# Performance work log

Hardware: AMD Instinct MI355X
Metric: run time of the kernel (lower is better)

## Reference

```python
import jax, jax.numpy as jnp
import numpy as np

D_MODEL = 256
NHEAD = 8
HEAD_DIM = D_MODEL // NHEAD
EPS_ATTN = 1e-6
EPS_LN = 1e-5


def layer_norm(x, g, b):
    mu = jnp.mean(x, axis=-1, keepdims=True)
    var = jnp.mean(jnp.square(x - mu), axis=-1, keepdims=True)
    return (x - mu) * jax.lax.rsqrt(var + EPS_LN) * g + b


def setup_inputs() -> dict:
    key = jax.random.key(0)
    ks = jax.random.split(key, 9)
    N, L, S = 8, 8192, 8192
    d = D_MODEL
    sc = 1.0 / np.sqrt(d)
    return {
        "x": jax.random.normal(ks[0], (N, L, d), dtype=jnp.float32),
        "source": jax.random.normal(ks[1], (N, S, d), dtype=jnp.float32),
        "Wq": jax.random.normal(ks[2], (d, d), dtype=jnp.float32) * sc,
        "Wk": jax.random.normal(ks[3], (d, d), dtype=jnp.float32) * sc,
        "Wv": jax.random.normal(ks[4], (d, d), dtype=jnp.float32) * sc,
        "Wm": jax.random.normal(ks[5], (d, d), dtype=jnp.float32) * sc,
        "W1": jax.random.normal(ks[6], (2 * d, d), dtype=jnp.float32) * (1.0 / np.sqrt(2 * d)),
        "W2": jax.random.normal(ks[7], (d, d), dtype=jnp.float32) * sc,
        "g1": jnp.ones((d,), jnp.float32),
        "b1": jnp.zeros((d,), jnp.float32),
        "g2": jnp.ones((d,), jnp.float32),
        "b2": jnp.zeros((d,), jnp.float32),
    }


def linear_attention(q, k, v):
    # q: [N,L,H,D], k,v: [N,S,H,D]
    Q = jax.nn.elu(q) + 1.0
    K = jax.nn.elu(k) + 1.0
    S = v.shape[1]
    v = v / S
    KV = jnp.einsum('nshd,nshv->nhdv', K, v)          # [N,H,D,D]
    Z = 1.0 / (jnp.einsum('nlhd,nhd->nlh', Q, K.sum(axis=1)) + EPS_ATTN)
    out = jnp.einsum('nlhd,nhdv,nlh->nlhv', Q, KV, Z) * S
    return out


def reference(x, source, Wq, Wk, Wv, Wm, W1, W2, g1, b1, g2, b2):
    N, L, _ = x.shape
    q = (x @ Wq).reshape(N, L, NHEAD, HEAD_DIM)
    k = (source @ Wk).reshape(N, -1, NHEAD, HEAD_DIM)
    v = (source @ Wv).reshape(N, -1, NHEAD, HEAD_DIM)
    msg = linear_attention(q, k, v).reshape(N, L, D_MODEL)
    msg = layer_norm(msg @ Wm, g1, b1)
    msg = jnp.concatenate([x, msg], axis=2)
    msg = jax.nn.relu(msg @ W1) @ W2
    msg = layer_norm(msg, g2, b2)
    return x + msg
```

## Files before the change

### kernel.cpp

```cpp
#include <hip/hip_runtime.h>

typedef __attribute__((ext_vector_type(4))) float f32x4;
typedef __attribute__((ext_vector_type(8))) short short8;
typedef __attribute__((ext_vector_type(4))) unsigned short us4;
typedef __attribute__((ext_vector_type(8))) unsigned short us8;

#define D_MODEL 256
#define SEQ 8192L
#define NBATCH 8
#define TOTROWS 65536L

__device__ inline unsigned short f2bf(float f){
  unsigned int u = __float_as_uint(f);
  u += 0x7fffu + ((u >> 16) & 1u);
  return (unsigned short)(u >> 16);
}
__device__ inline float bf2f(unsigned short h){
  return __uint_as_float(((unsigned int)h) << 16);
}
__device__ inline f32x4 mfma16(short8 a, short8 b, f32x4 c){
  return __builtin_amdgcn_mfma_f32_16x16x32_bf16(a, b, c, 0, 0, 0);
}
__device__ inline us8 pack8(f32x4 a, f32x4 b){
  us8 o;
  o[0]=f2bf(a[0]); o[1]=f2bf(a[1]); o[2]=f2bf(a[2]); o[3]=f2bf(a[3]);
  o[4]=f2bf(b[0]); o[5]=f2bf(b[1]); o[6]=f2bf(b[2]); o[7]=f2bf(b[3]);
  return o;
}

__global__ void prep_weights(const float* __restrict__ Wq, const float* __restrict__ Wk,
                             const float* __restrict__ Wv, const float* __restrict__ Wm,
                             const float* __restrict__ W1, const float* __restrict__ W2,
                             unsigned short* __restrict__ WT){
  int o = blockIdx.x * 256 + threadIdx.x;
  int m = o >> 16, rem = o & 65535, n = rem >> 8, k = rem & 255;
  const float* s;
  switch(m){
    case 0: s = Wq; break;
    case 1: s = Wk; break;
    case 2: s = Wv; break;
    case 3: s = Wm; break;
    case 4: s = W1; break;
    case 5: s = W1 + 65536; break;
    default: s = W2; break;
  }
  WT[o] = f2bf(s[k * 256 + n]);
}

__global__ __launch_bounds__(256) void kv_proj(
    const float* __restrict__ src, const unsigned short* __restrict__ WT,
    unsigned short* __restrict__ Kw, unsigned short* __restrict__ Vw)
{
  __shared__ unsigned short As[128][40];
  __shared__ unsigned short Bs[128][40];
  const int t = threadIdx.x, lane = t & 63, wid = t >> 6;
  const int l16 = lane & 15, g4 = lane >> 4;
  const int wr = (wid >> 1) * 64, wc = (wid & 1) * 64;
  const int mb = blockIdx.x, nb = blockIdx.y;
  const long rowbase = (long)mb * 128;
  const unsigned short* Wsl = WT + (nb < 2 ? 1 : 2) * 65536 + (nb & 1) * 128 * 256;
  const int rA = t >> 1, cA = (t & 1) * 16;

  f32x4 acc[4][4] = {};
  for(int kb = 0; kb < 256; kb += 32){
    {
      const float* g = src + (rowbase + rA) * 256 + kb + cA;
      f32x4 v0 = *(const f32x4*)g;
      f32x4 v1 = *(const f32x4*)(g + 4);
      f32x4 v2 = *(const f32x4*)(g + 8);
      f32x4 v3 = *(const f32x4*)(g + 12);
      *(us8*)&As[rA][cA]     = pack8(v0, v1);
      *(us8*)&As[rA][cA + 8] = pack8(v2, v3);
      const unsigned short* wb = Wsl + rA * 256 + kb + cA;
      *(us8*)&Bs[rA][cA]     = *(const us8*)wb;
      *(us8*)&Bs[rA][cA + 8] = *(const us8*)(wb + 8);
    }
    __syncthreads();
    short8 afr[4], bfr[4];
    #pragma unroll
    for(int mi = 0; mi < 4; mi++) afr[mi] = *(const short8*)&As[wr + mi*16 + l16][g4*8];
    #pragma unroll
    for(int ni = 0; ni < 4; ni++) bfr[ni] = *(const short8*)&Bs[wc + ni*16 + l16][g4*8];
    #pragma unroll
    for(int mi = 0; mi < 4; mi++)
      #pragma unroll
      for(int ni = 0; ni < 4; ni++)
        acc[mi][ni] = mfma16(afr[mi], bfr[ni], acc[mi][ni]);
    __syncthreads();
  }

  const bool isK = nb < 2;
  unsigned short* dst = isK ? Kw : Vw;
  const int colbase = (nb & 1) * 128 + wc;
  #pragma unroll
  for(int mi = 0; mi < 4; mi++)
    #pragma unroll
    for(int ni = 0; ni < 4; ni++)
      #pragma unroll
      for(int rr = 0; rr < 4; rr++){
        long row = rowbase + wr + mi*16 + g4*4 + rr;
        int col = colbase + ni*16 + l16;
        float v = acc[mi][ni][rr];
        v = isK ? (v > 0.f ? v + 1.f : __expf(v)) : v * (1.f / 8192.f);
        dst[row * 256 + col] = f2bf(v);
      }
}

__global__ __launch_bounds__(256) void kv_acc(const unsigned short* __restrict__ Kw,
                                              const unsigned short* __restrict__ Vw,
                                              float* __restrict__ part){
  const int c = blockIdx.x;
  const int n = blockIdx.y;
  const int t = threadIdx.x;
  const int h = t >> 5, d = t & 31;
  const long base = ((long)n * SEQ + (long)c * 128) * 256;
  float acc[32];
  #pragma unroll
  for(int j = 0; j < 32; j++) acc[j] = 0.f;
  float ks = 0.f;
  for(int rr = 0; rr < 128; rr++){
    const unsigned short* Kr = Kw + base + (long)rr * 256;
    const unsigned short* Vr = Vw + base + (long)rr * 256;
    float kv = bf2f(Kr[h * 32 + d]);
    ks += kv;
    #pragma unroll
    for(int q = 0; q < 4; q++){
      us8 vv = *(const us8*)(Vr + h * 32 + q * 8);
      #pragma unroll
      for(int j = 0; j < 8; j++) acc[q*8 + j] += kv * bf2f(vv[j]);
    }
  }
  float* p = part + ((long)(n * 64 + c) * 33) * 256;
  #pragma unroll
  for(int v = 0; v < 32; v++) p[v * 256 + t] = acc[v];
  p[32 * 256 + t] = ks;
}

__global__ void kv_red(const float* __restrict__ part, float* __restrict__ KVws){
  const int v = blockIdx.x;
  const int n = blockIdx.y;
  const int t = threadIdx.x;
  float s = 0.f;
  for(int c = 0; c < 64; c++) s += part[((long)(n * 64 + c) * 33 + v) * 256 + t];
  KVws[((long)n * 33 + v) * 256 + t] = s;
}

__global__ __launch_bounds__(256) void attn_kern(
    const float* __restrict__ x, const unsigned short* __restrict__ WT,
    const float* __restrict__ KVws, const float* __restrict__ g1,
    const float* __restrict__ b1, unsigned short* __restrict__ msgln)
{
  __shared__ unsigned short As[64][40];
  __shared__ unsigned short Bu[256][40];
  __shared__ float zs[64][8];
  __shared__ float ksl[256];
  __shared__ unsigned short R[64][264];

  const int t = threadIdx.x, lane = t & 63, wid = t >> 6;
  const int l16 = lane & 15, g4 = lane >> 4;
  const int wc = wid * 64;
  const int mb = blockIdx.x;
  const long rowbase = (long)mb * 64;
  const int n = mb >> 7;
  const int rS = t >> 2, cS = (t & 3) * 8;

  f32x4 acc[4][4] = {};
  {
    const unsigned short* wq = WT;
    for(int kb = 0; kb < 256; kb += 32){
      const float* g = x + (rowbase + rS) * 256 + kb + cS;
      f32x4 v0 = *(const f32x4*)g;
      f32x4 v1 = *(const f32x4*)(g + 4);
      *(us8*)&As[rS][cS] = pack8(v0, v1);
      const unsigned short* wb = wq + t * 256 + kb;
      *(us8*)&Bu[t][0]  = *(const us8*)(wb);
      *(us8*)&Bu[t][8]  = *(const us8*)(wb + 8);
      *(us8*)&Bu[t][16] = *(const us8*)(wb + 16);
      *(us8*)&Bu[t][24] = *(const us8*)(wb + 24);
      __syncthreads();
      short8 afr[4], bfr[4];
      #pragma unroll
      for(int mi = 0; mi < 4; mi++) afr[mi] = *(const short8*)&As[mi*16 + l16][g4*8];
      #pragma unroll
      for(int ni = 0; ni < 4; ni++) bfr[ni] = *(const short8*)&Bu[wc + ni*16 + l16][g4*8];
      #pragma unroll
      for(int mi = 0; mi < 4; mi++)
        #pragma unroll
        for(int ni = 0; ni < 4; ni++)
          acc[mi][ni] = mfma16(afr[mi], bfr[ni], acc[mi][ni]);
      __syncthreads();
    }
  }

  #pragma unroll
  for(int mi = 0; mi < 4; mi++)
    #pragma unroll
    for(int ni = 0; ni < 4; ni++)
      #pragma unroll
      for(int rr = 0; rr < 4; rr++){
        float v = acc[mi][ni][rr];
        v = v > 0.f ? v + 1.f : __expf(v);
        R[mi*16 + g4*4 + rr][wc + ni*16 + l16] = f2bf(v);
      }

  {
    const float* kvn = KVws + (long)n * 33 * 256;
    const int vv = t & 31, hh = t >> 5;
    #pragma unroll
    for(int d = 0; d < 32; d += 4){
      f32x4 w = *(const f32x4*)(kvn + vv * 256 + hh * 32 + d);
      us4 o; o[0]=f2bf(w[0]); o[1]=f2bf(w[1]); o[2]=f2bf(w[2]); o[3]=f2bf(w[3]);
      *(us4*)&Bu[t][d] = o;
    }
    ksl[t] = kvn[32 * 256 + t];
  }
  __syncthreads();

  #pragma unroll
  for(int pp = 0; pp < 2; pp++){
    int p = t + pp * 256;
    int row = p >> 3, h = p & 7;
    float s = 0.f;
    #pragma unroll
    for(int d = 0; d < 32; d++) s += bf2f(R[row][h*32 + d]) * ksl[h*32 + d];
    zs[row][h] = 1.f / (s + 1e-6f);
  }
  __syncthreads();

  f32x4 acc2[4][4];
  #pragma unroll
  for(int ni = 0; ni < 4; ni++){
    const int cb = wc + ni * 16;
    const int h = cb >> 5;
    short8 b = *(const short8*)&Bu[cb + l16][g4*8];
    #pragma unroll
    for(int mi = 0; mi < 4; mi++){
      short8 a = *(const short8*)&R[mi*16 + l16][h*32 + g4*8];
      f32x4 zz = {0.f, 0.f, 0.f, 0.f};
      acc2[mi][ni] = mfma16(a, b, zz);
    }
  }
  #pragma unroll
  for(int mi = 0; mi < 4; mi++)
    #pragma unroll
    for(int ni = 0; ni < 4; ni++){
      const int h = (wc + ni * 16) >> 5;
      #pragma unroll
      for(int rr = 0; rr < 4; rr++){
        int row = mi*16 + g4*4 + rr;
        acc2[mi][ni][rr] *= zs[row][h] * 8192.f;
      }
    }
  __syncthreads();
  #pragma unroll
  for(int mi = 0; mi < 4; mi++)
    #pragma unroll
    for(int ni = 0; ni < 4; ni++)
      #pragma unroll
      for(int rr = 0; rr < 4; rr++)
        R[mi*16 + g4*4 + rr][wc + ni*16 + l16] = f2bf(acc2[mi][ni][rr]);
  __syncthreads();

  f32x4 acc3[4][4] = {};
  {
    const unsigned short* wm = WT + 3 * 65536;
    for(int kb = 0; kb < 256; kb += 32){
      const unsigned short* wb = wm + t * 256 + kb;
      *(us8*)&Bu[t][0]  = *(const us8*)(wb);
      *(us8*)&Bu[t][8]  = *(const us8*)(wb + 8);
      *(us8*)&Bu[t][16] = *(const us8*)(wb + 16);
      *(us8*)&Bu[t][24] = *(const us8*)(wb + 24);
      __syncthreads();
      short8 afr[4], bfr[4];
      #pragma unroll
      for(int mi = 0; mi < 4; mi++) afr[mi] = *(const short8*)&R[mi*16 + l16][kb + g4*8];
      #pragma unroll
      for(int ni = 0; ni < 4; ni++) bfr[ni] = *(const short8*)&Bu[wc + ni*16 + l16][g4*8];
      #pragma unroll
      for(int mi = 0; mi < 4; mi++)
        #pragma unroll
        for(int ni = 0; ni < 4; ni++)
          acc3[mi][ni] = mfma16(afr[mi], bfr[ni], acc3[mi][ni]);
      __syncthreads();
    }
  }

  #pragma unroll
  for(int mi = 0; mi < 4; mi++)
    #pragma unroll
    for(int ni = 0; ni < 4; ni++)
      #pragma unroll
      for(int rr = 0; rr < 4; rr++)
        R[mi*16 + g4*4 + rr][wc + ni*16 + l16] = f2bf(acc3[mi][ni][rr]);
  __syncthreads();

  {
    int row = t >> 2, q = t & 3;
    float s = 0.f, ss = 0.f;
    #pragma unroll
    for(int j8 = 0; j8 < 8; j8++){
      us8 vv = *(const us8*)&R[row][q*64 + j8*8];
      #pragma unroll
      for(int e = 0; e < 8; e++){ float v = bf2f(vv[e]); s += v; ss += v * v; }
    }
    s  += __shfl_xor(s, 1);  ss += __shfl_xor(ss, 1);
    s  += __shfl_xor(s, 2);  ss += __shfl_xor(ss, 2);
    float mu  = s * (1.f / 256.f);
    float var = ss * (1.f / 256.f) - mu * mu;
    float rs  = rsqrtf(var + 1e-5f);
    unsigned short* orow = msgln + (rowbase + row) * 256 + q * 64;
    const float* g1p = g1 + q * 64;
    const float* b1p = b1 + q * 64;
    #pragma unroll
    for(int j8 = 0; j8 < 8; j8++){
      us8 vv = *(const us8*)&R[row][q*64 + j8*8];
      us8 o;
      #pragma unroll
      for(int e = 0; e < 8; e++){
        float v = (bf2f(vv[e]) - mu) * rs * g1p[j8*8 + e] + b1p[j8*8 + e];
        o[e] = f2bf(v);
      }
      *(us8*)(orow + j8*8) = o;
    }
  }
}

__global__ __launch_bounds__(256) void ffn_kern(
    const float* __restrict__ x, const unsigned short* __restrict__ WT,
    const unsigned short* __restrict__ msgln, const float* __restrict__ g2,
    const float* __restrict__ b2, float* __restrict__ out)
{
  __shared__ unsigned short As[64][40];
  __shared__ unsigned short Bs[256][40];
  __shared__ unsigned short R[64][264];
  const int t = threadIdx.x, lane = t & 63, wid = t >> 6;
  const int l16 = lane & 15, g4 = lane >> 4;
  const int wc = wid * 64;
  const long rowbase = (long)blockIdx.x * 64;
  const int rS = t >> 2, cS = (t & 3) * 8;

  f32x4 acc[4][4] = {};
  for(int it = 0; it < 16; it++){
    int kb = it * 32;
    if(it < 8){
      const float* g = x + (rowbase + rS) * 256 + kb + cS;
      f32x4 v0 = *(const f32x4*)g;
      f32x4 v1 = *(const f32x4*)(g + 4);
      *(us8*)&As[rS][cS] = pack8(v0, v1);
    } else {
      const unsigned short* g = msgln + (rowbase + rS) * 256 + (kb & 255) + cS;
      *(us8*)&As[rS][cS] = *(const us8*)g;
    }
    const unsigned short* wsl = WT + (it < 8 ? 4 : 5) * 65536 + t * 256 + (kb & 255);
    *(us8*)&Bs[t][0]  = *(const us8*)(wsl);
    *(us8*)&Bs[t][8]  = *(const us8*)(wsl + 8);
    *(us8*)&Bs[t][16] = *(const us8*)(wsl + 16);
    *(us8*)&Bs[t][24] = *(const us8*)(wsl + 24);
    __syncthreads();
    short8 afr[4], bfr[4];
    #pragma unroll
    for(int mi = 0; mi < 4; mi++) afr[mi] = *(const short8*)&As[mi*16 + l16][g4*8];
    #pragma unroll
    for(int ni = 0; ni < 4; ni++) bfr[ni] = *(const short8*)&Bs[wc + ni*16 + l16][g4*8];
    #pragma unroll
    for(int mi = 0; mi < 4; mi++)
      #pragma unroll
      for(int ni = 0; ni < 4; ni++)
        acc[mi][ni] = mfma16(afr[mi], bfr[ni], acc[mi][ni]);
    __syncthreads();
  }

  #pragma unroll
  for(int mi = 0; mi < 4; mi++)
    #pragma unroll
    for(int ni = 0; ni < 4; ni++)
      #pragma unroll
      for(int rr = 0; rr < 4; rr++){
        float v = acc[mi][ni][rr];
        R[mi*16 + g4*4 + rr][wc + ni*16 + l16] = f2bf(v > 0.f ? v : 0.f);
      }
  __syncthreads();

  f32x4 acc2[4][4] = {};
  {
    const unsigned short* w2 = WT + 6 * 65536;
    for(int kb = 0; kb < 256; kb += 32){
      const unsigned short* wb = w2 + t * 256 + kb;
      *(us8*)&Bs[t][0]  = *(const us8*)(wb);
      *(us8*)&Bs[t][8]  = *(const us8*)(wb + 8);
      *(us8*)&Bs[t][16] = *(const us8*)(wb + 16);
      *(us8*)&Bs[t][24] = *(const us8*)(wb + 24);
      __syncthreads();
      short8 afr[4], bfr[4];
      #pragma unroll
      for(int mi = 0; mi < 4; mi++) afr[mi] = *(const short8*)&R[mi*16 + l16][kb + g4*8];
      #pragma unroll
      for(int ni = 0; ni < 4; ni++) bfr[ni] = *(const short8*)&Bs[wc + ni*16 + l16][g4*8];
      #pragma unroll
      for(int mi = 0; mi < 4; mi++)
        #pragma unroll
        for(int ni = 0; ni < 4; ni++)
          acc2[mi][ni] = mfma16(afr[mi], bfr[ni], acc2[mi][ni]);
      __syncthreads();
    }
  }

  #pragma unroll
  for(int mi = 0; mi < 4; mi++)
    #pragma unroll
    for(int ni = 0; ni < 4; ni++)
      #pragma unroll
      for(int rr = 0; rr < 4; rr++)
        R[mi*16 + g4*4 + rr][wc + ni*16 + l16] = f2bf(acc2[mi][ni][rr]);
  __syncthreads();

  {
    int row = t >> 2, q = t & 3;
    float s = 0.f, ss = 0.f;
    #pragma unroll
    for(int j8 = 0; j8 < 8; j8++){
      us8 vv = *(const us8*)&R[row][q*64 + j8*8];
      #pragma unroll
      for(int e = 0; e < 8; e++){ float v = bf2f(vv[e]); s += v; ss += v * v; }
    }
    s  += __shfl_xor(s, 1);  ss += __shfl_xor(ss, 1);
    s  += __shfl_xor(s, 2);  ss += __shfl_xor(ss, 2);
    float mu  = s * (1.f / 256.f);
    float var = ss * (1.f / 256.f) - mu * mu;
    float rs  = rsqrtf(var + 1e-5f);
    const float* xr = x + (rowbase + row) * 256 + q * 64;
    float* orow = out + (rowbase + row) * 256 + q * 64;
    const float* g2p = g2 + q * 64;
    const float* b2p = b2 + q * 64;
    #pragma unroll
    for(int j4 = 0; j4 < 16; j4++){
      f32x4 xv = *(const f32x4*)(xr + j4 * 4);
      f32x4 o;
      #pragma unroll
      for(int e = 0; e < 4; e++){
        int idx = j4 * 4 + e;
        float v = (bf2f(R[row][q*64 + idx]) - mu) * rs * g2p[idx] + b2p[idx];
        o[e] = xv[e] + v;
      }
      *(f32x4*)(orow + j4 * 4) = o;
    }
  }
}

extern "C" void kernel_launch(void* const* d_in, const int* in_sizes, int n_in,
                              void* d_out, int out_size, void* d_ws, size_t ws_size,
                              hipStream_t stream)
{
  const float* x   = (const float*)d_in[0];
  const float* src = (const float*)d_in[1];
  const float* Wq  = (const float*)d_in[2];
  const float* Wk  = (const float*)d_in[3];
  const float* Wv  = (const float*)d_in[4];
  const float* Wm  = (const float*)d_in[5];
  const float* W1  = (const float*)d_in[6];
  const float* W2  = (const float*)d_in[7];
  const float* g1  = (const float*)d_in[8];
  const float* b1  = (const float*)d_in[9];
  const float* g2  = (const float*)d_in[10];
  const float* b2  = (const float*)d_in[11];

  char* ws = (char*)d_ws;
  unsigned short* WT   = (unsigned short*)(ws);
  unsigned short* Kw   = (unsigned short*)(ws + (1ul << 20));
  unsigned short* msgl = Kw;
  unsigned short* Vw   = (unsigned short*)(ws + (1ul << 20) + 33554432ul);
  float* part          = (float*)(ws + (1ul << 20) + 2ul * 33554432ul);
  float* KVws          = (float*)(ws + (1ul << 20) + 2ul * 33554432ul + 17301504ul);

  prep_weights<<<1792, 256, 0, stream>>>(Wq, Wk, Wv, Wm, W1, W2, WT);
  kv_proj<<<dim3(512, 4), 256, 0, stream>>>(src, WT, Kw, Vw);
  kv_acc<<<dim3(64, 8), 256, 0, stream>>>(Kw, Vw, part);
  kv_red<<<dim3(33, 8), 256, 0, stream>>>(part, KVws);
  attn_kern<<<1024, 256, 0, stream>>>(x, WT, KVws, g1, b1, msgl);
  ffn_kern<<<1024, 256, 0, stream>>>(x, WT, msgl, g2, b2, (float*)d_out);
}
```

Baseline: 452.8 us.

## Pre-convert inputs to bf16 and stage GEMM tiles via direct global-to-LDS loads

Adds a standalone kernel that converts source and x from fp32 to bf16 once. The projection, attention and FFN kernels then load A and B tiles with global_load_lds, which writes directly into unpadded LDS instead of passing through registers. This removes the repeated per-block fp32 loading and conversion, and the register round trip on tile staging. The cost is an extra fp32 read plus bf16 write pass over both inputs, possible LDS bank conflicts now that the padding is gone, and a workspace remap that reuses one region for srcb, part and xb.

Result: faster. 415.8 us (-8.2%).

```diff
diff --git a/kernel.cpp b/kernel.cpp
--- a/kernel.cpp
+++ b/kernel.cpp
@@ -26,6 +26,23 @@
   o[0]=f2bf(a[0]); o[1]=f2bf(a[1]); o[2]=f2bf(a[2]); o[3]=f2bf(a[3]);
   o[4]=f2bf(b[0]); o[5]=f2bf(b[1]); o[6]=f2bf(b[2]); o[7]=f2bf(b[3]);
   return o;
+}
+__device__ inline void gl16(const unsigned short* g, unsigned short* lds){
+  __builtin_amdgcn_global_load_lds(
+      (const __attribute__((address_space(1))) unsigned int*)g,
+      (__attribute__((address_space(3))) unsigned int*)lds, 16, 0, 0);
+}
+
+__global__ __launch_bounds__(256) void conv_f32_to_bf16(
+    const float* __restrict__ s, unsigned short* __restrict__ d){
+  const long N = TOTROWS * 256 / 8;
+  for(long c = (long)blockIdx.x * 256 + threadIdx.x; c < N;
+      c += (long)gridDim.x * 256){
+    long off = c * 8;
+    f32x4 v0 = *(const f32x4*)(s + off);
+    f32x4 v1 = *(const f32x4*)(s + off + 4);
+    *(us8*)(d + off) = pack8(v0, v1);
+  }
 }
 
 __global__ void prep_weights(const float* __restrict__ Wq, const float* __restrict__ Wk,
@@ -48,32 +65,26 @@
 }
 
 __global__ __launch_bounds__(256) void kv_proj(
-    const float* __restrict__ src, const unsigned short* __restrict__ WT,
+    const unsigned short* __restrict__ srcb, const unsigned short* __restrict__ WT,
     unsigned short* __restrict__ Kw, unsigned short* __restrict__ Vw)
 {
-  __shared__ unsigned short As[128][40];
-  __shared__ unsigned short Bs[128][40];
+  __shared__ unsigned short As[128][32];
+  __shared__ unsigned short Bs[128][32];
   const int t = threadIdx.x, lane = t & 63, wid = t >> 6;
   const int l16 = lane & 15, g4 = lane >> 4;
   const int wr = (wid >> 1) * 64, wc = (wid & 1) * 64;
   const int mb = blockIdx.x, nb = blockIdx.y;
   const long rowbase = (long)mb * 128;
   const unsigned short* Wsl = WT + (nb < 2 ? 1 : 2) * 65536 + (nb & 1) * 128 * 256;
-  const int rA = t >> 1, cA = (t & 1) * 16;
+  const int sr = lane >> 2, sc = (lane & 3) * 8;
 
   f32x4 acc[4][4] = {};
   for(int kb = 0; kb < 256; kb += 32){
-    {
-      const float* g = src + (rowbase + rA) * 256 + kb + cA;
-      f32x4 v0 = *(const f32x4*)g;
-      f32x4 v1 = *(const f32x4*)(g + 4);
-      f32x4 v2 = *(const f32x4*)(g + 8);
-      f32x4 v3 = *(const f32x4*)(g + 12);
-      *(us8*)&As[rA][cA]     = pack8(v0, v1);
-      *(us8*)&As[rA][cA + 8] = pack8(v2, v3);
-      const unsigned short* wb = Wsl + rA * 256 + kb + cA;
-      *(us8*)&Bs[rA][cA]     = *(const us8*)wb;
-      *(us8*)&Bs[rA][cA + 8] = *(const us8*)(wb + 8);
+    #pragma unroll
+    for(int j = 0; j < 2; j++){
+      int r0 = wid * 32 + j * 16;
+      gl16(srcb + (rowbase + r0 + sr) * 256 + kb + sc, &As[r0][0]);
+      gl16(Wsl  + (long)(r0 + sr) * 256 + kb + sc,     &Bs[r0][0]);
     }
     __syncthreads();
     short8 afr[4], bfr[4];
@@ -146,12 +157,12 @@
 }
 
 __global__ __launch_bounds__(256) void attn_kern(
-    const float* __restrict__ x, const unsigned short* __restrict__ WT,
+    const unsigned short* __restrict__ xb, const unsigned short* __restrict__ WT,
     const float* __restrict__ KVws, const float* __restrict__ g1,
     const float* __restrict__ b1, unsigned short* __restrict__ msgln)
 {
-  __shared__ unsigned short As[64][40];
-  __shared__ unsigned short Bu[256][40];
+  __shared__ unsigned short As[64][32];
+  __shared__ unsigned short Bu[256][32];
   __shared__ float zs[64][8];
   __shared__ float ksl[256];
   __shared__ unsigned short R[64][264];
@@ -162,21 +173,18 @@
   const int mb = blockIdx.x;
   const long rowbase = (long)mb * 64;
   const int n = mb >> 7;
-  const int rS = t >> 2, cS = (t & 3) * 8;
+  const int sr = lane >> 2, sc = (lane & 3) * 8;
 
   f32x4 acc[4][4] = {};
   {
     const unsigned short* wq = WT;
     for(int kb = 0; kb < 256; kb += 32){
-      const float* g = x + (rowbase + rS) * 256 + kb + cS;
-      f32x4 v0 = *(const f32x4*)g;
-      f32x4 v1 = *(const f32x4*)(g + 4);
-      *(us8*)&As[rS][cS] = pack8(v0, v1);
-      const unsigned short* wb = wq + t * 256 + kb;
-      *(us8*)&Bu[t][0]  = *(const us8*)(wb);
-      *(us8*)&Bu[t][8]  = *(const us8*)(wb + 8);
-      *(us8*)&Bu[t][16] = *(const us8*)(wb + 16);
-      *(us8*)&Bu[t][24] = *(const us8*)(wb + 24);
+      gl16(xb + (rowbase + wid*16 + sr) * 256 + kb + sc, &As[wid*16][0]);
+      #pragma unroll
+      for(int j = 0; j < 4; j++){
+        int r0 = wid * 64 + j * 16;
+        gl16(wq + (long)(r0 + sr) * 256 + kb + sc, &Bu[r0][0]);
+      }
       __syncthreads();
       short8 afr[4], bfr[4];
       #pragma unroll
@@ -265,11 +273,11 @@
   {
     const unsigned short* wm = WT + 3 * 65536;
     for(int kb = 0; kb < 256; kb += 32){
-      const unsigned short* wb = wm + t * 256 + kb;
-      *(us8*)&Bu[t][0]  = *(const us8*)(wb);
-      *(us8*)&Bu[t][8]  = *(const us8*)(wb + 8);
-      *(us8*)&Bu[t][16] = *(const us8*)(wb + 16);
-      *(us8*)&Bu[t][24] = *(const us8*)(wb + 24);
+      #pragma unroll
+      for(int j = 0; j < 4; j++){
+        int r0 = wid * 64 + j * 16;
+        gl16(wm + (long)(r0 + sr) * 256 + kb + sc, &Bu[r0][0]);
+      }
       __syncthreads();
       short8 afr[4], bfr[4];
       #pragma unroll
@@ -326,36 +334,31 @@
 }
 
 __global__ __launch_bounds__(256) void ffn_kern(
-    const float* __restrict__ x, const unsigned short* __restrict__ WT,
+    const float* __restrict__ x, const unsigned short* __restrict__ xb,
+    const unsigned short* __restrict__ WT,
     const unsigned short* __restrict__ msgln, const float* __restrict__ g2,
     const float* __restrict__ b2, float* __restrict__ out)
 {
-  __shared__ unsigned short As[64][40];
-  __shared__ unsigned short Bs[256][40];
+  __shared__ unsigned short As[64][32];
+  __shared__ unsigned short Bs[256][32];
   __shared__ unsigned short R[64][264];
   const int t = threadIdx.x, lane = t & 63, wid = t >> 6;
   const int l16 = lane & 15, g4 = lane >> 4;
   const int wc = wid * 64;
   const long rowbase = (long)blockIdx.x * 64;
-  const int rS = t >> 2, cS = (t & 3) * 8;
+  const int sr = lane >> 2, sc = (lane & 3) * 8;
 
   f32x4 acc[4][4] = {};
   for(int it = 0; it < 16; it++){
-    int kb = it * 32;
-    if(it < 8){
-      const float* g = x + (rowbase + rS) * 256 + kb + cS;
-      f32x4 v0 = *(const f32x4*)g;
-      f32x4 v1 = *(const f32x4*)(g + 4);
-      *(us8*)&As[rS][cS] = pack8(v0, v1);
-    } else {
-      const unsigned short* g = msgln + (rowbase + rS) * 256 + (kb & 255) + cS;
-      *(us8*)&As[rS][cS] = *(const us8*)g;
-    }
-    const unsigned short* wsl = WT + (it < 8 ? 4 : 5) * 65536 + t * 256 + (kb & 255);
-    *(us8*)&Bs[t][0]  = *(const us8*)(wsl);
-    *(us8*)&Bs[t][8]  = *(const us8*)(wsl + 8);
-    *(us8*)&Bs[t][16] = *(const us8*)(wsl + 16);
-    *(us8*)&Bs[t][24] = *(const us8*)(wsl + 24);
+    int kb = (it & 7) * 32;
+    const unsigned short* asrc = (it < 8) ? xb : msgln;
+    gl16(asrc + (rowbase + wid*16 + sr) * 256 + kb + sc, &As[wid*16][0]);
+    const unsigned short* wsl = WT + (it < 8 ? 4 : 5) * 65536;
+    #pragma unroll
+    for(int j = 0; j < 4; j++){
+      int r0 = wid * 64 + j * 16;
+      gl16(wsl + (long)(r0 + sr) * 256 + kb + sc, &Bs[r0][0]);
+    }
     __syncthreads();
     short8 afr[4], bfr[4];
     #pragma unroll
@@ -385,11 +388,11 @@
   {
     const unsigned short* w2 = WT + 6 * 65536;
     for(int kb = 0; kb < 256; kb += 32){
-      const unsigned short* wb = w2 + t * 256 + kb;
-      *(us8*)&Bs[t][0]  = *(const us8*)(wb);
-      *(us8*)&Bs[t][8]  = *(const us8*)(wb + 8);
-      *(us8*)&Bs[t][16] = *(const us8*)(wb + 16);
-      *(us8*)&Bs[t][24] = *(const us8*)(wb + 24);
+      #pragma unroll
+      for(int j = 0; j < 4; j++){
+        int r0 = wid * 64 + j * 16;
+        gl16(w2 + (long)(r0 + sr) * 256 + kb + sc, &Bs[r0][0]);
+      }
       __syncthreads();
       short8 afr[4], bfr[4];
       #pragma unroll
@@ -466,16 +469,20 @@
 
   char* ws = (char*)d_ws;
   unsigned short* WT   = (unsigned short*)(ws);
-  unsigned short* Kw   = (unsigned short*)(ws + (1ul << 20));
+  unsigned short* srcb = (unsigned short*)(ws + (1ul  << 20));
+  float*          part = (float*)         (ws + (1ul  << 20));
+  unsigned short* xb   = (unsigned short*)(ws + (1ul  << 20));
+  unsigned short* Kw   = (unsigned short*)(ws + (33ul << 20));
   unsigned short* msgl = Kw;
-  unsigned short* Vw   = (unsigned short*)(ws + (1ul << 20) + 33554432ul);
-  float* part          = (float*)(ws + (1ul << 20) + 2ul * 33554432ul);
-  float* KVws          = (float*)(ws + (1ul << 20) + 2ul * 33554432ul + 17301504ul);
+  unsigned short* Vw   = (unsigned short*)(ws + (65ul << 20));
+  float*          KVws = (float*)         (ws + (97ul << 20));
 
   prep_weights<<<1792, 256, 0, stream>>>(Wq, Wk, Wv, Wm, W1, W2, WT);
-  kv_proj<<<dim3(512, 4), 256, 0, stream>>>(src, WT, Kw, Vw);
+  conv_f32_to_bf16<<<2048, 256, 0, stream>>>(src, srcb);
+  kv_proj<<<dim3(512, 4), 256, 0, stream>>>(srcb, WT, Kw, Vw);
   kv_acc<<<dim3(64, 8), 256, 0, stream>>>(Kw, Vw, part);
   kv_red<<<dim3(33, 8), 256, 0, stream>>>(part, KVws);
-  attn_kern<<<1024, 256, 0, stream>>>(x, WT, KVws, g1, b1, msgl);
-  ffn_kern<<<1024, 256, 0, stream>>>(x, WT, msgl, g2, b2, (float*)d_out);
-}
+  conv_f32_to_bf16<<<2048, 256, 0, stream>>>(x, xb);
+  attn_kern<<<1024, 256, 0, stream>>>(xb, WT, KVws, g1, b1, msgl);
+  ffn_kern<<<1024, 256, 0, stream>>>(x, xb, WT, msgl, g2, b2, (float*)d_out);
+}
```
